# Kernel tuning notes

Hardware: AMD Instinct MI355X
Metric: run time of the kernel (lower is better)

Reference implementation:

```python
import jax, jax.numpy as jnp
import numpy as np

# Scatter2Operator config (matches init_kwargs)
NUM_HEADS = 16   # dims[2] / glob_size
GLOB_SIZE = 64
HEAD_SIZE = 64   # dims[2] / num_heads


def setup_inputs() -> dict:
    key = jax.random.key(0)
    ks = jax.random.split(key, 6)
    B, N, G, D0, D2 = 8, 4096, 64, 1024, 1024
    scale = 0.02
    return {
        "x0": jax.random.normal(ks[0], (B, G, D0), jnp.float32),
        "x2": jax.random.normal(ks[1], (B, N, D2), jnp.float32),
        "Wk": jax.random.normal(ks[2], (NUM_HEADS * GLOB_SIZE, D2), jnp.float32) * scale,
        "Wp": jax.random.normal(ks[3], (NUM_HEADS * HEAD_SIZE, D0), jnp.float32) * scale,
        "Wo": jax.random.normal(ks[4], (D2, NUM_HEADS * HEAD_SIZE), jnp.float32) * scale,
        "bo": jnp.zeros((D2,), jnp.float32),
    }


def reference(x0, x2, Wk, Wp, Wo, bo):
    # x2: [B, N, D2] -> kernel scores; x0: [B, G, D0] -> premise values.
    B, N, _ = x2.shape
    H, G, Dh = NUM_HEADS, GLOB_SIZE, HEAD_SIZE
    # kernel = softmax over glob slots (dropout is identity in eval mode)
    k = jnp.einsum('bnd,kd->bnk', x2, Wk).reshape(B, N, H, G)
    k = jax.nn.softmax(k, axis=-1)                      # [B, N, H, G]
    # premise projection: [B, G, H, Dh]
    p = jnp.einsum('bgd,kd->bgk', x0, Wp).reshape(B, G, H, Dh)
    # attention-like gather over the G global slots, per head
    pred = jnp.einsum('bnhg,bghd->bnhd', k, p)          # [B, N, H, Dh]
    pred = pred.reshape(B, N, H * Dh)
    # writer linear (with bias)
    return jnp.einsum('bnk,dk->bnd', pred, Wo) + bo
```

## Files before the change

kernel.cpp:

```cpp
#include <hip/hip_runtime.h>


using bf16x8 = __attribute__((ext_vector_type(8))) __bf16;
using f32x4  = __attribute__((ext_vector_type(4))) float;

__device__ __forceinline__ unsigned short f2b(float f) {
  unsigned u = __float_as_uint(f);
  u += 0x7fffu + ((u >> 16) & 1u);
  return (unsigned short)(u >> 16);
}

__global__ void cvt_f32_bf16(const float* __restrict__ in, unsigned short* __restrict__ out, int n4) {
  int i = blockIdx.x * blockDim.x + threadIdx.x;
  int stride = gridDim.x * blockDim.x;
  for (; i < n4; i += stride) {
    float4 v = reinterpret_cast<const float4*>(in)[i];
    ushort4 o;
    o.x = f2b(v.x); o.y = f2b(v.y); o.z = f2b(v.z); o.w = f2b(v.w);
    reinterpret_cast<ushort4*>(out)[i] = o;
  }
}

#define GLOAD_LDS(gsrc, ldst) __builtin_amdgcn_global_load_lds(                 \
    (const __attribute__((address_space(1))) unsigned int*)(gsrc),              \
    (__attribute__((address_space(3))) unsigned int*)(ldst), 16, 0, 0)

__device__ __forceinline__ void glds16(const unsigned short* g, unsigned ldsoff) {
  asm volatile("s_mov_b32 m0, %0\n\t"
               "global_load_lds_dwordx4 %1, off"
               :: "s"(ldsoff), "v"(g) : "memory");
}

#define BM 128
#define BN 128
#define BK 32

template<int EPI>
__launch_bounds__(256)
__global__ void gemm_bt(const unsigned short* __restrict__ A,
                        const unsigned short* __restrict__ B,
                        void* __restrict__ Cv,
                        const float* __restrict__ bias,
                        int M, int N, int K, int lda, int ldb, int ldc,
                        int batch2,
                        long sA1, long sA2, long sB1, long sB2, long sC1, long sC2)
{
  __shared__ __align__(16) unsigned short As[BM * BK];
  __shared__ __align__(16) unsigned short Bs[BN * BK];

  const int z  = blockIdx.z;
  const int z1 = z / batch2, z2 = z - z1 * batch2;
  const unsigned short* Ab = A + z1 * sA1 + z2 * sA2;
  const unsigned short* Bb = B + z1 * sB1 + z2 * sB2;
  const long cbase = z1 * sC1 + z2 * sC2;

  const int tid  = threadIdx.x;
  const int lane = tid & 63;
  const int wid  = tid >> 6;
  const int wr   = (wid >> 1) * 64;
  const int wc   = (wid & 1) * 64;
  const int brow = blockIdx.x * BM;
  const int bcol = blockIdx.y * BN;
  const int lr   = lane & 15;
  const int ko   = (lane >> 4) * 8;

  f32x4 acc[4][4] = {};

  const int t1  = tid + 256;
  const int r0  = tid >> 2, kc0 = (tid & 3) * 8;
  const int r1  = t1 >> 2,  kc1 = (t1 & 3) * 8;
  int ar0 = brow + r0; if (ar0 >= M) ar0 = M - 1;
  int ar1 = brow + r1; if (ar1 >= M) ar1 = M - 1;
  int br0 = bcol + r0; if (br0 >= N) br0 = N - 1;
  int br1 = bcol + r1; if (br1 >= N) br1 = N - 1;
  const unsigned short* a0p = Ab + (long)ar0 * lda + kc0;
  const unsigned short* a1p = Ab + (long)ar1 * lda + kc1;
  const unsigned short* b0p = Bb + (long)br0 * ldb + kc0;
  const unsigned short* b1p = Bb + (long)br1 * ldb + kc1;

  for (int kt = 0; kt < K; kt += BK) {
    __syncthreads();
    GLOAD_LDS(a0p + kt, &As[tid * 8]);
    GLOAD_LDS(a1p + kt, &As[t1 * 8]);
    GLOAD_LDS(b0p + kt, &Bs[tid * 8]);
    GLOAD_LDS(b1p + kt, &Bs[t1 * 8]);
    __syncthreads();

    bf16x8 af[4], bfr[4];
#pragma unroll
    for (int m = 0; m < 4; ++m)
      af[m] = *reinterpret_cast<const bf16x8*>(&As[(wr + m * 16 + lr) * BK + ko]);
#pragma unroll
    for (int n = 0; n < 4; ++n)
      bfr[n] = *reinterpret_cast<const bf16x8*>(&Bs[(wc + n * 16 + lr) * BK + ko]);
#pragma unroll
    for (int m = 0; m < 4; ++m)
#pragma unroll
      for (int n = 0; n < 4; ++n)
        acc[m][n] = __builtin_amdgcn_mfma_f32_16x16x32_bf16(af[m], bfr[n], acc[m][n], 0, 0, 0);
  }

  const int rowb = brow + wr + (lane >> 4) * 4;
  const int colb = bcol + wc + lr;

  if (EPI == 1) {
    float* C = (float*)Cv + cbase;
#pragma unroll
    for (int n = 0; n < 4; ++n) {
      int col = colb + n * 16;
      if (col >= N) continue;
      float bv = bias ? bias[col] : 0.0f;
#pragma unroll
      for (int m = 0; m < 4; ++m)
#pragma unroll
        for (int r = 0; r < 4; ++r) {
          int row = rowb + m * 16 + r;
          if (row < M) C[(long)row * ldc + col] = acc[m][n][r] + bv;
        }
    }
  } else {
    unsigned short* C = (unsigned short*)Cv + cbase;
#pragma unroll
    for (int n = 0; n < 4; ++n) {
      int col = colb + n * 16;
      if (col >= N) continue;
#pragma unroll
      for (int m = 0; m < 4; ++m)
#pragma unroll
        for (int r = 0; r < 4; ++r) {
          int row = rowb + m * 16 + r;
          if (row < M) C[(long)row * ldc + col] = f2b(acc[m][n][r]);
        }
    }
  }
}


#define BARRIER() __builtin_amdgcn_s_barrier()
#define VMC4()   asm volatile("s_waitcnt vmcnt(4)" ::: "memory")
#define VMC0()   asm volatile("s_waitcnt vmcnt(0)" ::: "memory")

template<int EPI, int BATCHED>
__launch_bounds__(512)
__global__ void gemm256(const unsigned short* __restrict__ A,
                        const unsigned short* __restrict__ B,
                        void* __restrict__ Cv,
                        const float* __restrict__ bias,
                        int K, int lda, int ldb, int ldc,
                        long sA, long sB, long sC)
{
  extern __shared__ __align__(16) char smem[];

  const int tid  = threadIdx.x;
  const int lane = tid & 63, wid = tid >> 6;
  const int wm = wid >> 2, wn = wid & 3;
  const int lr = lane & 15, hi = lane >> 4;
  const int swz  = (lane & 7) << 4;
  const int prow = lane >> 3;
  const int pxor = ((lane & 7) ^ prow) * 8;

  int bx, by; long abase = 0, bbase = 0, cbase = 0;
  if (BATCHED) {
    const int bid = blockIdx.x;
    const int z = bid & 7, idx = bid >> 3;
    bx = idx & 15; by = idx >> 4;
    abase = (long)z * sA; bbase = (long)z * sB; cbase = (long)z * sC;
  } else {
    const int bid = blockIdx.x;
    const int lin = (bid & 7) * 64 + (bid >> 3);
    bx = lin >> 2; by = lin & 3;
  }
  const int brow = bx * 256, bcol = by * 256;

  const unsigned short* __restrict__ Ab = A + abase;
  const unsigned short* __restrict__ Bb = B + bbase;

  unsigned short* ldsA[2] = { (unsigned short*)(smem),
                              (unsigned short*)(smem + 65536) };
  unsigned short* ldsB[2] = { (unsigned short*)(smem + 32768),
                              (unsigned short*)(smem + 98304) };

  const unsigned ldsbase =
      __builtin_amdgcn_readfirstlane((unsigned)(unsigned long long)smem);

  const long ldaL = lda, ldbL = ldb;

  auto stageA = [&](int buf, int h, int kt) {
    const unsigned short* s = Ab + (long)(brow + h * 128 + wid * 8 + prow) * ldaL + kt + pxor;
    unsigned d = ldsbase + (unsigned)(buf * 65536 + h * 16384 + wid * 1024);
    glds16(s, __builtin_amdgcn_readfirstlane(d));
    glds16(s + 64 * ldaL, __builtin_amdgcn_readfirstlane(d + 8192u));
  };
  auto stageB = [&](int buf, int h, int kt) {
    const unsigned short* s = Bb + (long)(bcol + h * 128 + wid * 8 + prow) * ldbL + kt + pxor;
    unsigned d = ldsbase + (unsigned)(32768 + buf * 65536 + h * 16384 + wid * 1024);
    glds16(s, __builtin_amdgcn_readfirstlane(d));
    glds16(s + 64 * ldbL, __builtin_amdgcn_readfirstlane(d + 8192u));
  };

  bf16x8 afr[4][2], bfr[4][2];
  auto ldA_ = [&](int buf, int mh) {
    const unsigned short* base = ldsA[buf];
#pragma unroll
    for (int mi = 0; mi < 4; ++mi) {
      const int row = wm * 128 + mh * 64 + mi * 16 + lr;
#pragma unroll
      for (int ks = 0; ks < 2; ++ks) {
        const int cb = (ks * 64 + hi * 16) ^ swz;
        afr[mi][ks] = *(const bf16x8*)(base + row * 64 + (cb >> 1));
      }
    }
  };
  auto ldB_ = [&](int buf, int nh) {
    const unsigned short* base = ldsB[buf];
#pragma unroll
    for (int ni = 0; ni < 2; ++ni) {
      const int row = wn * 64 + nh * 32 + ni * 16 + lr;
#pragma unroll
      for (int ks = 0; ks < 2; ++ks) {
        const int cb = (ks * 64 + hi * 16) ^ swz;
        bfr[nh * 2 + ni][ks] = *(const bf16x8*)(base + row * 64 + (cb >> 1));
      }
    }
  };

  f32x4 acc[8][4] = {};
  auto mmaQ = [&](int mh, int nh) {
    __builtin_amdgcn_s_setprio(1);
#pragma unroll
    for (int ks = 0; ks < 2; ++ks)
#pragma unroll
      for (int mi = 0; mi < 4; ++mi)
#pragma unroll
        for (int ni = 0; ni < 2; ++ni)
          acc[mh * 4 + mi][nh * 2 + ni] = __builtin_amdgcn_mfma_f32_16x16x32_bf16(
              afr[mi][ks], bfr[nh * 2 + ni][ks], acc[mh * 4 + mi][nh * 2 + ni], 0, 0, 0);
    __builtin_amdgcn_s_setprio(0);
  };

  stageB(0, 0, 0); stageB(0, 1, 0); stageA(0, 0, 0); stageA(0, 1, 0);
  stageB(1, 0, 64); stageB(1, 1, 64);
  VMC4(); BARRIER();

  const int NI = K >> 7;
#pragma unroll 1
  for (int i = 0; i < NI; ++i) {
    const int kt1 = i * 128 + 64;
    int kt2 = i * 128 + 128; if (kt2 >= K) kt2 -= K;
    int kt3 = i * 128 + 192; if (kt3 >= K) kt3 -= K;

    ldA_(0, 0); ldB_(0, 0); ldB_(0, 1); stageA(1, 0, kt1);
    BARRIER(); mmaQ(0, 0); BARRIER();
    stageA(1, 1, kt1);
    BARRIER(); mmaQ(0, 1); BARRIER();
    ldA_(0, 1); stageB(0, 0, kt2);
    BARRIER(); mmaQ(1, 0); BARRIER();
    stageB(0, 1, kt2); VMC4();
    BARRIER(); mmaQ(1, 1); BARRIER();
    ldA_(1, 0); ldB_(1, 0); ldB_(1, 1); stageA(0, 0, kt2);
    BARRIER(); mmaQ(0, 0); BARRIER();
    stageA(0, 1, kt2);
    BARRIER(); mmaQ(0, 1); BARRIER();
    ldA_(1, 1); stageB(1, 0, kt3);
    BARRIER(); mmaQ(1, 0); BARRIER();
    stageB(1, 1, kt3); VMC4();
    BARRIER(); mmaQ(1, 1); BARRIER();
  }
  VMC0();

  const int rowb = brow + wm * 128 + hi * 4;
  const int colb = bcol + wn * 64 + lr;

  if (EPI == 2) {
    unsigned short* C = (unsigned short*)Cv + cbase;
#pragma unroll
    for (int m = 0; m < 8; ++m) {
#pragma unroll
      for (int r = 0; r < 4; ++r) {
        float v0 = acc[m][0][r], v1 = acc[m][1][r], v2 = acc[m][2][r], v3 = acc[m][3][r];
        float mx = fmaxf(fmaxf(v0, v1), fmaxf(v2, v3));
        mx = fmaxf(mx, __shfl_xor(mx, 1));
        mx = fmaxf(mx, __shfl_xor(mx, 2));
        mx = fmaxf(mx, __shfl_xor(mx, 4));
        mx = fmaxf(mx, __shfl_xor(mx, 8));
        float e0 = __expf(v0 - mx), e1 = __expf(v1 - mx);
        float e2 = __expf(v2 - mx), e3 = __expf(v3 - mx);
        float s = e0 + e1 + e2 + e3;
        s += __shfl_xor(s, 1);
        s += __shfl_xor(s, 2);
        s += __shfl_xor(s, 4);
        s += __shfl_xor(s, 8);
        float inv = 1.0f / s;
        unsigned short* cp = C + (long)(rowb + m * 16 + r) * ldc + colb;
        cp[0]  = f2b(e0 * inv);
        cp[16] = f2b(e1 * inv);
        cp[32] = f2b(e2 * inv);
        cp[48] = f2b(e3 * inv);
      }
    }
  } else {
    float* C = (float*)Cv + cbase;
#pragma unroll
    for (int n = 0; n < 4; ++n) {
      const int col = colb + n * 16;
      const float bv = bias[col];
#pragma unroll
      for (int m = 0; m < 8; ++m)
#pragma unroll
        for (int r = 0; r < 4; ++r)
          C[(long)(rowb + m * 16 + r) * ldc + col] = acc[m][n][r] + bv;
    }
  }
}

extern "C" void kernel_launch(void* const* d_in, const int* in_sizes, int n_in,
                              void* d_out, int out_size, void* d_ws, size_t ws_size,
                              hipStream_t stream) {
  (void)in_sizes; (void)n_in; (void)out_size; (void)ws_size;
  const float* x0 = (const float*)d_in[0];
  const float* x2 = (const float*)d_in[1];
  const float* Wk = (const float*)d_in[2];
  const float* Wp = (const float*)d_in[3];
  const float* Wo = (const float*)d_in[4];
  const float* bo = (const float*)d_in[5];
  float* out = (float*)d_out;

  const long Bz = 8, Nn = 4096, Gg = 64, Dd = 1024;
  const long MN = Bz * Nn;

  char* ws = (char*)d_ws;
  size_t off = 0;
  auto alloc = [&](size_t bytes) {
    size_t cur = off;
    off = (cur + bytes + 255) & ~(size_t)255;
    return (unsigned short*)(ws + cur);
  };
  unsigned short* x2b = alloc(MN * Dd * 2);
  unsigned short* kb  = alloc(MN * Dd * 2);
  unsigned short* Wkb = alloc(Dd * Dd * 2);
  unsigned short* Wpb = alloc(Dd * Dd * 2);
  unsigned short* Wob = alloc(Dd * Dd * 2);
  unsigned short* x0b = alloc(Bz * Gg * Dd * 2);
  unsigned short* Pb  = alloc(Bz * Gg * Dd * 2);
  unsigned short* Qtb = alloc(Bz * Dd * Dd * 2);

  hipFuncSetAttribute(reinterpret_cast<const void*>(gemm256<2, 0>),
                      hipFuncAttributeMaxDynamicSharedMemorySize, 131072);
  hipFuncSetAttribute(reinterpret_cast<const void*>(gemm256<1, 1>),
                      hipFuncAttributeMaxDynamicSharedMemorySize, 131072);

  cvt_f32_bf16<<<dim3(4096), dim3(256), 0, stream>>>(x2, x2b, (int)(MN * Dd / 4));
  cvt_f32_bf16<<<dim3(512),  dim3(256), 0, stream>>>(x0, x0b, (int)(Bz * Gg * Dd / 4));
  cvt_f32_bf16<<<dim3(1024), dim3(256), 0, stream>>>(Wk, Wkb, (int)(Dd * Dd / 4));
  cvt_f32_bf16<<<dim3(1024), dim3(256), 0, stream>>>(Wp, Wpb, (int)(Dd * Dd / 4));
  cvt_f32_bf16<<<dim3(1024), dim3(256), 0, stream>>>(Wo, Wob, (int)(Dd * Dd / 4));

  gemm_bt<0><<<dim3(4, 8, 1), dim3(256), 0, stream>>>(
      x0b, Wpb, Pb, nullptr, 512, 1024, 1024, 1024, 1024, 1024,
      1, 0, 0, 0, 0, 0, 0);

  gemm256<2, 0><<<dim3(512, 1, 1), dim3(512), 131072, stream>>>(
      x2b, Wkb, kb, nullptr, 1024, 1024, 1024, 1024, 0, 0, 0);

  gemm_bt<0><<<dim3(8, 1, 128), dim3(256), 0, stream>>>(
      Wob, Pb, Qtb, nullptr, 1024, 64, 64, 1024, 1024, 1024,
      16, 0, 64, 65536, 64, 1048576, 64);

  gemm256<1, 1><<<dim3(512, 1, 1), dim3(512), 131072, stream>>>(
      kb, Qtb, (void*)out, bo, 1024, 1024, 1024, 1024,
      (long)4096 * 1024, (long)1024 * 1024, (long)4096 * 1024);
}
```

Measured before the change: 250.9 us.

## Restructure GEMM pipeline into uniform LDS-read/MMA phases with smaller fragment registers

Reworks the main loop of the 256-tile GEMM into eight uniform phases. Each phase loads a quarter of the A and B fragments from LDS, issues the next tile's global-to-LDS loads, waits on lgkmcnt, then runs 16 MFMAs at raised priority. Fragment registers drop from 4x2 B fragments to 2x2 per phase, which lowers register pressure. The prefetch now stays one K-tile ahead instead of staggering across B ahead of A, and each buffer waits for vmcnt(0). In exchange, LDS fragment reloads increase and there is less load/compute overlap depth.

```diff
diff --git a/kernel.cpp b/kernel.cpp
--- a/kernel.cpp
+++ b/kernel.cpp
@@ -137,7 +137,6 @@
 
 
 #define BARRIER() __builtin_amdgcn_s_barrier()
-#define VMC4()   asm volatile("s_waitcnt vmcnt(4)" ::: "memory")
 #define VMC0()   asm volatile("s_waitcnt vmcnt(0)" ::: "memory")
 
 template<int EPI, int BATCHED>
@@ -198,8 +197,8 @@
     glds16(s + 64 * ldbL, __builtin_amdgcn_readfirstlane(d + 8192u));
   };
 
-  bf16x8 afr[4][2], bfr[4][2];
-  auto ldA_ = [&](int buf, int mh) {
+  bf16x8 aq[4][2], bq[2][2];
+  auto ldAq = [&](int buf, int mh) {
     const unsigned short* base = ldsA[buf];
 #pragma unroll
     for (int mi = 0; mi < 4; ++mi) {
@@ -207,11 +206,11 @@
 #pragma unroll
       for (int ks = 0; ks < 2; ++ks) {
         const int cb = (ks * 64 + hi * 16) ^ swz;
-        afr[mi][ks] = *(const bf16x8*)(base + row * 64 + (cb >> 1));
+        aq[mi][ks] = *(const bf16x8*)(base + row * 64 + (cb >> 1));
       }
     }
   };
-  auto ldB_ = [&](int buf, int nh) {
+  auto ldBq = [&](int buf, int nh) {
     const unsigned short* base = ldsB[buf];
 #pragma unroll
     for (int ni = 0; ni < 2; ++ni) {
@@ -219,14 +218,13 @@
 #pragma unroll
       for (int ks = 0; ks < 2; ++ks) {
         const int cb = (ks * 64 + hi * 16) ^ swz;
-        bfr[nh * 2 + ni][ks] = *(const bf16x8*)(base + row * 64 + (cb >> 1));
+        bq[ni][ks] = *(const bf16x8*)(base + row * 64 + (cb >> 1));
       }
     }
   };
 
   f32x4 acc[8][4] = {};
-  auto mmaQ = [&](int mh, int nh) {
-    __builtin_amdgcn_s_setprio(1);
+  auto mma16 = [&](int mh, int nh) {
 #pragma unroll
     for (int ks = 0; ks < 2; ++ks)
 #pragma unroll
@@ -234,37 +232,39 @@
 #pragma unroll
         for (int ni = 0; ni < 2; ++ni)
           acc[mh * 4 + mi][nh * 2 + ni] = __builtin_amdgcn_mfma_f32_16x16x32_bf16(
-              afr[mi][ks], bfr[nh * 2 + ni][ks], acc[mh * 4 + mi][nh * 2 + ni], 0, 0, 0);
-    __builtin_amdgcn_s_setprio(0);
-  };
-
-  stageB(0, 0, 0); stageB(0, 1, 0); stageA(0, 0, 0); stageA(0, 1, 0);
-  stageB(1, 0, 64); stageB(1, 1, 64);
-  VMC4(); BARRIER();
+              aq[mi][ks], bq[ni][ks], acc[mh * 4 + mi][nh * 2 + ni], 0, 0, 0);
+  };
+
+  stageA(0, 0, 0); stageB(0, 0, 0); stageB(0, 1, 0); stageA(0, 1, 0);
+  VMC0(); BARRIER();
 
   const int NI = K >> 7;
 #pragma unroll 1
   for (int i = 0; i < NI; ++i) {
-    const int kt1 = i * 128 + 64;
-    int kt2 = i * 128 + 128; if (kt2 >= K) kt2 -= K;
-    int kt3 = i * 128 + 192; if (kt3 >= K) kt3 -= K;
-
-    ldA_(0, 0); ldB_(0, 0); ldB_(0, 1); stageA(1, 0, kt1);
-    BARRIER(); mmaQ(0, 0); BARRIER();
-    stageA(1, 1, kt1);
-    BARRIER(); mmaQ(0, 1); BARRIER();
-    ldA_(0, 1); stageB(0, 0, kt2);
-    BARRIER(); mmaQ(1, 0); BARRIER();
-    stageB(0, 1, kt2); VMC4();
-    BARRIER(); mmaQ(1, 1); BARRIER();
-    ldA_(1, 0); ldB_(1, 0); ldB_(1, 1); stageA(0, 0, kt2);
-    BARRIER(); mmaQ(0, 0); BARRIER();
-    stageA(0, 1, kt2);
-    BARRIER(); mmaQ(0, 1); BARRIER();
-    ldA_(1, 1); stageB(1, 0, kt3);
-    BARRIER(); mmaQ(1, 0); BARRIER();
-    stageB(1, 1, kt3); VMC4();
-    BARRIER(); mmaQ(1, 1); BARRIER();
+    const int ktb1 = i * 128 + 64;
+    int ktb0 = i * 128 + 128; if (ktb0 >= K) ktb0 -= K;
+
+#define PHASE(BUF, MH, NH, STAGES, WAIT)                        \
+    ldAq(BUF, MH); ldBq(BUF, NH);                               \
+    STAGES;                                                     \
+    BARRIER();                                                  \
+    asm volatile("s_waitcnt lgkmcnt(0)" ::: "memory");          \
+    __builtin_amdgcn_sched_barrier(0);                          \
+    __builtin_amdgcn_s_setprio(1);                              \
+    mma16(MH, NH);                                              \
+    __builtin_amdgcn_s_setprio(0);                              \
+    WAIT;                                                       \
+    BARRIER();
+
+    PHASE(0, 0, 0, { stageA(1, 0, ktb1); stageB(1, 0, ktb1); }, )
+    PHASE(0, 0, 1, { stageB(1, 1, ktb1); stageA(1, 1, ktb1); }, )
+    PHASE(0, 1, 0, , )
+    PHASE(0, 1, 1, , VMC0())
+    PHASE(1, 0, 0, { stageA(0, 0, ktb0); stageB(0, 0, ktb0); }, )
+    PHASE(1, 0, 1, { stageB(0, 1, ktb0); stageA(0, 1, ktb0); }, )
+    PHASE(1, 1, 0, , )
+    PHASE(1, 1, 1, , VMC0())
+#undef PHASE
   }
   VMC0();
 
```

Result: slower. 267.3 us (+6.5%).
